# Kernel tuning notes

Measured on AMD Instinct MI355X. Metric: run time of the kernel, lower is better.

The kernel has to match this reference:

```python
import jax, jax.numpy as jnp
import numpy as np

N, E, H, D_IN, L, G, T = 50000, 800000, 64, 64, 4, 128, 1

def _w(key, shape, fan_in):
    return jax.random.normal(key, shape, dtype=jnp.float32) / np.sqrt(fan_in)

def setup_inputs() -> dict:
    key = jax.random.key(0)
    ks = jax.random.split(key, 24)
    inp = {
        'x': jax.random.normal(ks[0], (N, D_IN), dtype=jnp.float32),
        'w': jax.random.normal(ks[1], (E, 1), dtype=jnp.float32),
        'src': jax.random.randint(ks[2], (E,), 0, N, dtype=jnp.int32),
        'dst': jax.random.randint(ks[3], (E,), 0, N, dtype=jnp.int32),
        'graph_id': jnp.sort(jax.random.randint(ks[4], (N,), 0, G, dtype=jnp.int32)),
        # input MLP (1 layer, last_activation None; SiLU applied in input_node_func)
        'W_in': _w(ks[5], (D_IN, H), D_IN), 'b_in': jnp.zeros((H,), jnp.float32),
        # per-layer message MLP: (2H+1 -> H -> H), SiLU mid and last
        'msg_W1': _w(ks[6], (L, 2 * H + 1, H), 2 * H + 1), 'msg_b1': jnp.zeros((L, H), jnp.float32),
        'msg_W2': _w(ks[7], (L, H, H), H), 'msg_b2': jnp.zeros((L, H), jnp.float32),
        # per-layer update MLP: (H -> H -> H), SiLU mid, last None
        'upd_W1': _w(ks[8], (L, H, H), H), 'upd_b1': jnp.zeros((L, H), jnp.float32),
        'upd_W2': _w(ks[9], (L, H, H), H), 'upd_b2': jnp.zeros((L, H), jnp.float32),
        # node-wise output MLP: (H -> H -> H), SiLU mid, last None
        'out_W1': _w(ks[10], (H, H), H), 'out_b1': jnp.zeros((H,), jnp.float32),
        'out_W2': _w(ks[11], (H, H), H), 'out_b2': jnp.zeros((H,), jnp.float32),
        # readout MLP: (3H -> H -> T), SiLU mid, last None
        'ro_W1': _w(ks[12], (3 * H, H), 3 * H), 'ro_b1': jnp.zeros((H,), jnp.float32),
        'ro_W2': _w(ks[13], (H, T), H), 'ro_b2': jnp.zeros((T,), jnp.float32),
    }
    return inp

def reference(x, w, src, dst, graph_id, W_in, b_in, msg_W1, msg_b1, msg_W2, msg_b2,
              upd_W1, upd_b1, upd_W2, upd_b2, out_W1, out_b1, out_W2, out_b2,
              ro_W1, ro_b1, ro_W2, ro_b2):
    silu = jax.nn.silu
    f = silu(x @ W_in + b_in)                                   # [N, H]
    sq = w * w                                                  # [E, 1]
    for l in range(L):
        mi = jnp.concatenate([f[src], f[dst], sq], axis=-1)     # [E, 2H+1]
        msg = silu(silu(mi @ msg_W1[l] + msg_b1[l]) @ msg_W2[l] + msg_b2[l])
        m = msg * jax.nn.sigmoid(msg)                           # gated message
        m_sum = jax.ops.segment_sum(m, dst, num_segments=N)     # scatter-sum to dst
        h_new = silu((m_sum + f) @ upd_W1[l] + upd_b1[l]) @ upd_W2[l] + upd_b2[l]
        f = h_new + f                                           # residual
    f = silu(f @ out_W1 + out_b1) @ out_W2 + out_b2             # node-wise output
    g_sum = jax.ops.segment_sum(f, graph_id, num_segments=G)
    cnt = jax.ops.segment_sum(jnp.ones((N, 1), f.dtype), graph_id, num_segments=G)
    g_mean = g_sum / jnp.maximum(cnt, 1.0)
    g_max = jax.ops.segment_max(f, graph_id, num_segments=G)
    readout = jnp.concatenate([g_sum, g_mean, g_max], axis=-1)  # [G, 3H]
    return silu(readout @ ro_W1 + ro_b1) @ ro_W2 + ro_b2        # [G, T]
```

## Files before the change

### kernel.cpp

```cpp
#include <hip/hip_runtime.h>

#define NN 50000
#define EE 800000
#define GG 128
#define LL 4
#define SCAN_B 196

typedef __bf16 bf16x8 __attribute__((ext_vector_type(8)));
typedef __bf16 bf16x4 __attribute__((ext_vector_type(4)));
typedef float  f32x4  __attribute__((ext_vector_type(4)));

__device__ __forceinline__ float silu_f(float x){
    float t = __builtin_amdgcn_exp2f(-1.44269504f * x);
    return x * __builtin_amdgcn_rcpf(1.0f + t);
}

__global__ __launch_bounds__(256) void pack_k(
        const float* __restrict__ msgW1, const float* __restrict__ msgW2,
        const float* __restrict__ updW1, const float* __restrict__ updW2,
        const float* __restrict__ outW1, const float* __restrict__ outW2,
        const float* __restrict__ W_in, __bf16* __restrict__ pk){
    int m = blockIdx.x;
    const float* src;
    if(m<20){
        int l=m/5, r=m%5;
        if(r==0)      src = msgW1 + (size_t)l*129*64;
        else if(r==1) src = msgW1 + (size_t)l*129*64 + 64*64;
        else if(r==2) src = msgW2 + (size_t)l*64*64;
        else if(r==3) src = updW1 + (size_t)l*64*64;
        else          src = updW2 + (size_t)l*64*64;
    } else if(m==20) src=outW1; else if(m==21) src=outW2; else src=W_in;
    __bf16* dst = pk + (size_t)m*4096;
    int tid=threadIdx.x;
    #pragma unroll
    for(int i=0;i<16;++i){
        int idx = tid*16+i;
        int frag = idx>>9, lane=(idx>>3)&63, j=idx&7;
        int s=frag>>2, ng=frag&3, q=lane>>4, nn=lane&15;
        dst[idx] = (__bf16)src[(32*s+8*q+j)*64 + 16*ng + nn];
    }
}
__device__ __forceinline__ bf16x8 ldfrag(const __bf16* pk, int s, int ng, int lane){
    return *(const bf16x8*)&pk[(((s*4+ng)*64 + lane))*8];
}

__global__ __launch_bounds__(256) void input_mfma(const float* __restrict__ x,
        const __bf16* __restrict__ pkW, const float* __restrict__ bg,
        const __bf16* __restrict__ pkXYa, const __bf16* __restrict__ pkXYb,
        const float* __restrict__ bXY,
        float* __restrict__ f, __bf16* __restrict__ XYout, int N){
    int tid=threadIdx.x, wid=tid>>6, lane=tid&63;
    int q=lane>>4, nn=lane&15;
    bf16x8 Bf[2][4];
    #pragma unroll
    for(int s=0;s<2;++s)
        #pragma unroll
        for(int ng=0;ng<4;++ng) Bf[s][ng]=ldfrag(pkW,s,ng,lane);
    float bias[4], bXYv[4];
    #pragma unroll
    for(int ng=0;ng<4;++ng){ bias[ng]=bg[16*ng+nn]; bXYv[ng]=bXY[16*ng+nn]; }

    __shared__ __align__(16) __bf16 sh1[4][16][72];

    int ntiles=(N+15)/16;
    int gw=gridDim.x*4;
    for(int t=blockIdx.x*4+wid; t<ntiles; t+=gw){
        int m=t*16+nn; int mc=(m<N)?m:(N-1);
        float4 a0=*(const float4*)&x[(size_t)mc*64 + 8*q];
        float4 a1=*(const float4*)&x[(size_t)mc*64 + 8*q + 4];
        float4 a2=*(const float4*)&x[(size_t)mc*64 + 32 + 8*q];
        float4 a3=*(const float4*)&x[(size_t)mc*64 + 32 + 8*q + 4];
        bf16x8 af0, af1;
        af0[0]=(__bf16)a0.x; af0[1]=(__bf16)a0.y; af0[2]=(__bf16)a0.z; af0[3]=(__bf16)a0.w;
        af0[4]=(__bf16)a1.x; af0[5]=(__bf16)a1.y; af0[6]=(__bf16)a1.z; af0[7]=(__bf16)a1.w;
        af1[0]=(__bf16)a2.x; af1[1]=(__bf16)a2.y; af1[2]=(__bf16)a2.z; af1[3]=(__bf16)a2.w;
        af1[4]=(__bf16)a3.x; af1[5]=(__bf16)a3.y; af1[6]=(__bf16)a3.z; af1[7]=(__bf16)a3.w;
        #pragma unroll
        for(int ng=0;ng<4;++ng){
            f32x4 acc; acc[0]=bias[ng]; acc[1]=bias[ng]; acc[2]=bias[ng]; acc[3]=bias[ng];
            acc=__builtin_amdgcn_mfma_f32_16x16x32_bf16(af0,Bf[0][ng],acc,0,0,0);
            acc=__builtin_amdgcn_mfma_f32_16x16x32_bf16(af1,Bf[1][ng],acc,0,0,0);
            #pragma unroll
            for(int r=0;r<4;++r){
                int row=t*16+4*q+r;
                float o=silu_f(acc[r]);
                if(row<N) f[(size_t)row*64+16*ng+nn]=o;
                sh1[wid][4*q+r][16*ng+nn]=(__bf16)o;
            }
        }
        asm volatile("" ::: "memory");
        bf16x8 a30=*(const bf16x8*)&sh1[wid][nn][8*q];
        bf16x8 a31=*(const bf16x8*)&sh1[wid][nn][32+8*q];
        #pragma unroll
        for(int ng=0;ng<8;++ng){
            const __bf16* pkx = (ng<4)? pkXYa : pkXYb;
            int g2 = ng&3;
            float bb = (ng<4)?0.f:bXYv[ng-4];
            f32x4 accx; accx[0]=bb; accx[1]=bb; accx[2]=bb; accx[3]=bb;
            accx=__builtin_amdgcn_mfma_f32_16x16x32_bf16(a30,ldfrag(pkx,0,g2,lane),accx,0,0,0);
            accx=__builtin_amdgcn_mfma_f32_16x16x32_bf16(a31,ldfrag(pkx,1,g2,lane),accx,0,0,0);
            #pragma unroll
            for(int r=0;r<4;++r){
                int row=t*16+4*q+r;
                if(row<N) XYout[(size_t)row*128 + 16*ng + nn]=(__bf16)accx[r];
            }
        }
        asm volatile("" ::: "memory");
    }
}

__global__ void hist_k(const int* __restrict__ dst, int* __restrict__ deg, int E){
    int e=blockIdx.x*blockDim.x+threadIdx.x;
    if(e<E) atomicAdd(&deg[dst[e]],1);
}

__global__ __launch_bounds__(256) void scan1_k(const int* __restrict__ deg, int* __restrict__ curs,
        int* __restrict__ bsum, int N){
    __shared__ int sv[256];
    int tid=threadIdx.x;
    int idx=blockIdx.x*256+tid;
    int v=(idx<N)?deg[idx]:0;
    sv[tid]=v; __syncthreads();
    #pragma unroll
    for(int off=1; off<256; off<<=1){
        int a=(tid>=off)?sv[tid-off]:0;
        __syncthreads(); sv[tid]+=a; __syncthreads();
    }
    if(idx<N) curs[idx]=sv[tid]-v;
    if(tid==255) bsum[blockIdx.x]=sv[255];
}
__global__ __launch_bounds__(256) void scan2_k(int* __restrict__ bsum, int B){
    __shared__ int sv[256];
    int tid=threadIdx.x;
    int v=(tid<B)?bsum[tid]:0;
    sv[tid]=v; __syncthreads();
    #pragma unroll
    for(int off=1; off<256; off<<=1){
        int a=(tid>=off)?sv[tid-off]:0;
        __syncthreads(); sv[tid]+=a; __syncthreads();
    }
    if(tid<B) bsum[tid]=sv[tid]-v;
}
__global__ __launch_bounds__(256) void scan3_k(int* __restrict__ curs, const int* __restrict__ bsum, int N){
    int idx=blockIdx.x*256+threadIdx.x;
    if(idx<N) curs[idx]+=bsum[blockIdx.x];
}

__global__ void fill_k(const int* __restrict__ src, const int* __restrict__ dst,
                       const float* __restrict__ w, int* __restrict__ cursor,
                       int4* __restrict__ meta, int E){
    int e=blockIdx.x*blockDim.x+threadIdx.x;
    if(e<E){
        int d=dst[e];
        int r=atomicAdd(&cursor[d],1);
        float ww=w[e];
        int4 v; v.x=src[e]; v.y=d; v.z=__float_as_int(ww*ww); v.w=0;
        meta[r]=v;
    }
}

__global__ __launch_bounds__(256) void edge_mfma6(
        const __bf16* __restrict__ XY, const int4* __restrict__ meta,
        const __bf16* __restrict__ pkW2,
        const float* __restrict__ W1, const float* __restrict__ b2,
        float* __restrict__ msum, int E){
    int tid=threadIdx.x, wid=tid>>6, lane=tid&63;
    int q=lane>>4, nn=lane&15;

    bf16x8 B2f[2][4];
    #pragma unroll
    for(int s=0;s<2;++s)
        #pragma unroll
        for(int ng=0;ng<4;++ng) B2f[s][ng]=ldfrag(pkW2,s,ng,lane);
    float w128lo[8], w128hi[8];
    #pragma unroll
    for(int j=0;j<8;++j){
        w128lo[j]=W1[128*64 + 8*q+j];
        w128hi[j]=W1[128*64 + 32+8*q+j];
    }
    float bias2[4];
    #pragma unroll
    for(int ng=0;ng<4;++ng) bias2[ng]=b2[16*ng+nn];

    __shared__ __align__(16) __bf16 sm16[4][32][68];
    int cpos = 4*(lane&15) + (lane>>4);

    int ntiles=E/32;
    int nw=gridDim.x*4;
    int chunk=(ntiles+nw-1)/nw;
    int wgl=blockIdx.x*4+wid;
    int t0=wgl*chunk, t1=t0+chunk; if(t1>ntiles) t1=ntiles;
    if(t0>=t1) return;

    int4 mv  = meta[(size_t)t0*32 + (lane&31)];
    int4 mvn = (t0+1<t1) ? meta[(size_t)(t0+1)*32 + (lane&31)] : mv;
    bf16x8 gx0lo,gx0hi,gy0lo,gy0hi,gx1lo,gx1hi,gy1lo,gy1hi;
    {
        int se0=__shfl(mv.x, nn,64),    de0=__shfl(mv.y, nn,64);
        int se1=__shfl(mv.x, 16+nn,64), de1=__shfl(mv.y, 16+nn,64);
        const __bf16* xp0=XY+(size_t)se0*128; const __bf16* yp0=XY+(size_t)de0*128+64;
        const __bf16* xp1=XY+(size_t)se1*128; const __bf16* yp1=XY+(size_t)de1*128+64;
        gx0lo=*(const bf16x8*)(xp0+8*q); gx0hi=*(const bf16x8*)(xp0+32+8*q);
        gy0lo=*(const bf16x8*)(yp0+8*q); gy0hi=*(const bf16x8*)(yp0+32+8*q);
        gx1lo=*(const bf16x8*)(xp1+8*q); gx1hi=*(const bf16x8*)(xp1+32+8*q);
        gy1lo=*(const bf16x8*)(yp1+8*q); gy1hi=*(const bf16x8*)(yp1+32+8*q);
    }
    int cur=__builtin_amdgcn_readlane(mv.y, 0);
    float vsum=0.f;

    for(int t=t0;t<t1;++t){
        int4 mv2 = mvn;
        if(t+2<t1) mv2 = meta[(size_t)(t+2)*32 + (lane&31)];

        int d_ = mv.y;
        float w2v = __int_as_float(mv.z);

        bf16x8 A0lo,A0hi,A1lo,A1hi;
        {
            float w2a = __shfl(w2v, nn, 64);
            float w2b = __shfl(w2v, 16+nn, 64);
            #pragma unroll
            for(int j=0;j<8;++j){
                A0lo[j]=(__bf16)silu_f((float)gx0lo[j] + (float)gy0lo[j] + w2a*w128lo[j]);
                A0hi[j]=(__bf16)silu_f((float)gx0hi[j] + (float)gy0hi[j] + w2a*w128hi[j]);
                A1lo[j]=(__bf16)silu_f((float)gx1lo[j] + (float)gy1lo[j] + w2b*w128lo[j]);
                A1hi[j]=(__bf16)silu_f((float)gx1hi[j] + (float)gy1hi[j] + w2b*w128hi[j]);
            }
        }
        if(t+1<t1){
            int se0=__shfl(mvn.x, nn,64),    de0=__shfl(mvn.y, nn,64);
            int se1=__shfl(mvn.x, 16+nn,64), de1=__shfl(mvn.y, 16+nn,64);
            const __bf16* xp0=XY+(size_t)se0*128; const __bf16* yp0=XY+(size_t)de0*128+64;
            const __bf16* xp1=XY+(size_t)se1*128; const __bf16* yp1=XY+(size_t)de1*128+64;
            gx0lo=*(const bf16x8*)(xp0+8*q); gx0hi=*(const bf16x8*)(xp0+32+8*q);
            gy0lo=*(const bf16x8*)(yp0+8*q); gy0hi=*(const bf16x8*)(yp0+32+8*q);
            gx1lo=*(const bf16x8*)(xp1+8*q); gx1hi=*(const bf16x8*)(xp1+32+8*q);
            gy1lo=*(const bf16x8*)(yp1+8*q); gy1hi=*(const bf16x8*)(yp1+32+8*q);
        }
        #pragma unroll
        for(int h=0;h<2;++h){
            bf16x8 alo = h ? A1lo : A0lo;
            bf16x8 ahi = h ? A1hi : A0hi;
            f32x4 acc2[4];
            #pragma unroll
            for(int ng=0;ng<4;++ng){ f32x4 c; c[0]=bias2[ng]; c[1]=bias2[ng]; c[2]=bias2[ng]; c[3]=bias2[ng]; acc2[ng]=c; }
            #pragma unroll
            for(int ng=0;ng<4;++ng){
                acc2[ng]=__builtin_amdgcn_mfma_f32_16x16x32_bf16(alo,B2f[0][ng],acc2[ng],0,0,0);
                acc2[ng]=__builtin_amdgcn_mfma_f32_16x16x32_bf16(ahi,B2f[1][ng],acc2[ng],0,0,0);
            }
            #pragma unroll
            for(int r=0;r<4;++r){
                bf16x4 pv;
                #pragma unroll
                for(int ng=0;ng<4;++ng) pv[ng]=(__bf16)silu_f(silu_f(acc2[ng][r]));
                *(bf16x4*)&sm16[wid][16*h+4*q+r][4*nn] = pv;
            }
        }
        asm volatile("" ::: "memory");
        {
            int dprev = __shfl(d_, (lane+63)&63, 64);
            unsigned long long bal = __ballot(lane>=1 && lane<32 && d_!=dprev);
            unsigned bmask = (unsigned)bal;
            int d0 = __builtin_amdgcn_readlane(d_, 0);
            if(d0 != cur) bmask |= 1u;
            #pragma unroll
            for(int r=0;r<32;++r){
                if(bmask & (1u<<r)){
                    atomicAdd(&msum[(size_t)cur*64+lane], vsum);
                    vsum=0.f;
                    cur=__builtin_amdgcn_readlane(d_, r);
                }
                vsum += (float)sm16[wid][r][cpos];
            }
        }
        asm volatile("" ::: "memory");
        mv = mvn; mvn = mv2;
    }
    atomicAdd(&msum[(size_t)cur*64+lane], vsum);
}

__global__ __launch_bounds__(256) void node_mfma(float* A, const float* F,
        const __bf16* __restrict__ pkW1, const float* __restrict__ b1,
        const __bf16* __restrict__ pkW2, const float* __restrict__ b2,
        float* __restrict__ out, int zeroA,
        const __bf16* __restrict__ pkXYa, const __bf16* __restrict__ pkXYb,
        const float* __restrict__ bXY, __bf16* __restrict__ XYout, int N){
    int tid=threadIdx.x, wid=tid>>6, lane=tid&63;
    int q=lane>>4, nn=lane&15;

    bf16x8 B1f[2][4], B2f[2][4];
    #pragma unroll
    for(int s=0;s<2;++s)
        #pragma unroll
        for(int ng=0;ng<4;++ng){ B1f[s][ng]=ldfrag(pkW1,s,ng,lane); B2f[s][ng]=ldfrag(pkW2,s,ng,lane); }
    float bias1[4], bias2[4];
    #pragma unroll
    for(int ng=0;ng<4;++ng){ bias1[ng]=b1[16*ng+nn]; bias2[ng]=b2[16*ng+nn]; }
    bool hasXY = (pkXYa != nullptr);
    float bXYv[4];
    #pragma unroll
    for(int j=0;j<4;++j) bXYv[j] = hasXY ? bXY[16*j+nn] : 0.f;

    __shared__ __align__(16) __bf16 sh1[4][16][72];
    __shared__ __align__(16) float sF[4][16][68];
    bool hasF = (F != nullptr);

    int ntiles=(N+15)/16;
    int gw=gridDim.x*4;
    for(int t=blockIdx.x*4+wid; t<ntiles; t+=gw){
        int m=t*16+nn;
        int mc=(m<N)?m:(N-1);
        float4 a0=*(const float4*)&A[(size_t)mc*64 + 8*q];
        float4 a1=*(const float4*)&A[(size_t)mc*64 + 8*q + 4];
        float4 a2=*(const float4*)&A[(size_t)mc*64 + 32 + 8*q];
        float4 a3=*(const float4*)&A[(size_t)mc*64 + 32 + 8*q + 4];
        if(hasF){
            float4 f0=*(const float4*)&F[(size_t)mc*64 + 8*q];
            float4 f1=*(const float4*)&F[(size_t)mc*64 + 8*q + 4];
            float4 f2_=*(const float4*)&F[(size_t)mc*64 + 32 + 8*q];
            float4 f3=*(const float4*)&F[(size_t)mc*64 + 32 + 8*q + 4];
            a0.x+=f0.x; a0.y+=f0.y; a0.z+=f0.z; a0.w+=f0.w;
            a1.x+=f1.x; a1.y+=f1.y; a1.z+=f1.z; a1.w+=f1.w;
            a2.x+=f2_.x; a2.y+=f2_.y; a2.z+=f2_.z; a2.w+=f2_.w;
            a3.x+=f3.x; a3.y+=f3.y; a3.z+=f3.z; a3.w+=f3.w;
            *(float4*)&sF[wid][nn][8*q]   = f0;
            *(float4*)&sF[wid][nn][8*q+4] = f1;
            *(float4*)&sF[wid][nn][32+8*q]   = f2_;
            *(float4*)&sF[wid][nn][32+8*q+4] = f3;
        }
        if(zeroA && m<N){
            float4 z; z.x=0.f; z.y=0.f; z.z=0.f; z.w=0.f;
            *(float4*)&A[(size_t)mc*64 + 8*q]      = z;
            *(float4*)&A[(size_t)mc*64 + 8*q + 4]  = z;
            *(float4*)&A[(size_t)mc*64 + 32 + 8*q] = z;
            *(float4*)&A[(size_t)mc*64 + 32 + 8*q + 4] = z;
        }
        bf16x8 af0, af1;
        af0[0]=(__bf16)a0.x; af0[1]=(__bf16)a0.y; af0[2]=(__bf16)a0.z; af0[3]=(__bf16)a0.w;
        af0[4]=(__bf16)a1.x; af0[5]=(__bf16)a1.y; af0[6]=(__bf16)a1.z; af0[7]=(__bf16)a1.w;
        af1[0]=(__bf16)a2.x; af1[1]=(__bf16)a2.y; af1[2]=(__bf16)a2.z; af1[3]=(__bf16)a2.w;
        af1[4]=(__bf16)a3.x; af1[5]=(__bf16)a3.y; af1[6]=(__bf16)a3.z; af1[7]=(__bf16)a3.w;

        f32x4 acc[4];
        #pragma unroll
        for(int ng=0;ng<4;++ng){ f32x4 c; c[0]=bias1[ng]; c[1]=bias1[ng]; c[2]=bias1[ng]; c[3]=bias1[ng]; acc[ng]=c; }
        #pragma unroll
        for(int ng=0;ng<4;++ng){
            acc[ng]=__builtin_amdgcn_mfma_f32_16x16x32_bf16(af0,B1f[0][ng],acc[ng],0,0,0);
            acc[ng]=__builtin_amdgcn_mfma_f32_16x16x32_bf16(af1,B1f[1][ng],acc[ng],0,0,0);
        }
        #pragma unroll
        for(int ng=0;ng<4;++ng)
            #pragma unroll
            for(int r=0;r<4;++r)
                sh1[wid][4*q+r][16*ng+nn]=(__bf16)silu_f(acc[ng][r]);
        asm volatile("" ::: "memory");
        bf16x8 a20=*(const bf16x8*)&sh1[wid][nn][8*q];
        bf16x8 a21=*(const bf16x8*)&sh1[wid][nn][32+8*q];
        f32x4 acc2[4];
        #pragma unroll
        for(int ng=0;ng<4;++ng){ f32x4 c; c[0]=bias2[ng]; c[1]=bias2[ng]; c[2]=bias2[ng]; c[3]=bias2[ng]; acc2[ng]=c; }
        #pragma unroll
        for(int ng=0;ng<4;++ng){
            acc2[ng]=__builtin_amdgcn_mfma_f32_16x16x32_bf16(a20,B2f[0][ng],acc2[ng],0,0,0);
            acc2[ng]=__builtin_amdgcn_mfma_f32_16x16x32_bf16(a21,B2f[1][ng],acc2[ng],0,0,0);
        }
        #pragma unroll
        for(int ng=0;ng<4;++ng)
            #pragma unroll
            for(int r=0;r<4;++r){
                int row=t*16+4*q+r;
                float o=acc2[ng][r];
                if(hasF) o += sF[wid][4*q+r][16*ng+nn];
                if(row<N) out[(size_t)row*64 + 16*ng + nn]=o;
                if(hasXY) sh1[wid][4*q+r][16*ng+nn]=(__bf16)o;
            }
        asm volatile("" ::: "memory");
        if(hasXY){
            bf16x8 a30=*(const bf16x8*)&sh1[wid][nn][8*q];
            bf16x8 a31=*(const bf16x8*)&sh1[wid][nn][32+8*q];
            #pragma unroll
            for(int ng=0;ng<8;++ng){
                const __bf16* pkx = (ng<4)? pkXYa : pkXYb;
                int g2 = ng&3;
                float bb = (ng<4)?0.f:bXYv[ng-4];
                f32x4 accx; accx[0]=bb; accx[1]=bb; accx[2]=bb; accx[3]=bb;
                accx=__builtin_amdgcn_mfma_f32_16x16x32_bf16(a30,ldfrag(pkx,0,g2,lane),accx,0,0,0);
                accx=__builtin_amdgcn_mfma_f32_16x16x32_bf16(a31,ldfrag(pkx,1,g2,lane),accx,0,0,0);
                #pragma unroll
                for(int r=0;r<4;++r){
                    int row=t*16+4*q+r;
                    if(row<N) XYout[(size_t)row*128 + 16*ng + nn]=(__bf16)accx[r];
                }
            }
        }
        asm volatile("" ::: "memory");
    }
}

__global__ __launch_bounds__(256) void readout_fused(const float* __restrict__ f2,
        const int* __restrict__ gid,
        const float* __restrict__ W1, const float* __restrict__ b1,
        const float* __restrict__ W2, const float* __restrict__ b2,
        float* __restrict__ out, int N, int G){
    __shared__ __align__(16) float sr[4][192];
    int tid=threadIdx.x, wid=tid>>6, lane=tid&63;
    int g=blockIdx.x*4+wid;
    if(g<G){
        int lo=0, hi=N;
        while(lo<hi){ int mid=(lo+hi)>>1; if(gid[mid]<g) lo=mid+1; else hi=mid; }
        int a=lo, b=N;
        while(a<b){ int mid=(a+b)>>1; if(gid[mid]<g+1) a=mid+1; else b=mid; }
        int n0=lo, n1=a;
        float s=0.f, mx=-__builtin_inff();
        int n=n0;
        for(; n+4<=n1; n+=4){
            float v0=f2[(size_t)(n+0)*64+lane];
            float v1=f2[(size_t)(n+1)*64+lane];
            float v2=f2[(size_t)(n+2)*64+lane];
            float v3=f2[(size_t)(n+3)*64+lane];
            s += (v0+v1)+(v2+v3);
            mx = fmaxf(mx, fmaxf(fmaxf(v0,v1), fmaxf(v2,v3)));
        }
        for(; n<n1; ++n){ float v=f2[(size_t)n*64+lane]; s+=v; mx=fmaxf(mx,v); }
        float c=(float)(n1-n0);
        float mean=s/fmaxf(c,1.0f);
        sr[wid][lane]=s; sr[wid][64+lane]=mean; sr[wid][128+lane]=mx;
    }
    __syncthreads();
    if(g<G){
        float h=b1[lane];
        for(int k=0;k<192;k+=4){
            float4 r4=*(const float4*)&sr[wid][k];
            h += r4.x*W1[(k+0)*64+lane] + r4.y*W1[(k+1)*64+lane]
               + r4.z*W1[(k+2)*64+lane] + r4.w*W1[(k+3)*64+lane];
        }
        h=silu_f(h);
        float p=h*W2[lane];
        #pragma unroll
        for(int off=32;off>0;off>>=1) p += __shfl_down(p, off, 64);
        if(lane==0) out[g]=p+b2[0];
    }
}

extern "C" void kernel_launch(void* const* d_in, const int* in_sizes, int n_in,
                              void* d_out, int out_size, void* d_ws, size_t ws_size,
                              hipStream_t stream){
    const float* x     = (const float*)d_in[0];
    const float* w     = (const float*)d_in[1];
    const int*   src   = (const int*)d_in[2];
    const int*   dst   = (const int*)d_in[3];
    const int*   gid   = (const int*)d_in[4];
    const float* W_in  = (const float*)d_in[5];
    const float* b_in  = (const float*)d_in[6];
    const float* msgW1 = (const float*)d_in[7];
    const float* msgb1 = (const float*)d_in[8];
    const float* msgW2 = (const float*)d_in[9];
    const float* msgb2 = (const float*)d_in[10];
    const float* updW1 = (const float*)d_in[11];
    const float* updb1 = (const float*)d_in[12];
    const float* updW2 = (const float*)d_in[13];
    const float* updb2 = (const float*)d_in[14];
    const float* outW1 = (const float*)d_in[15];
    const float* outb1 = (const float*)d_in[16];
    const float* outW2 = (const float*)d_in[17];
    const float* outb2 = (const float*)d_in[18];
    const float* roW1  = (const float*)d_in[19];
    const float* rob1  = (const float*)d_in[20];
    const float* roW2  = (const float*)d_in[21];
    const float* rob2  = (const float*)d_in[22];

    float*  f     = (float*)d_ws;
    float*  msum  = f + (size_t)NN*64;
    float*  f2    = msum;
    __bf16* XY    = (__bf16*)(msum + (size_t)NN*64);
    int4*   meta  = (int4*)(XY + (size_t)NN*128);
    __bf16* pk    = (__bf16*)(meta + EE);
    int*    deg   = (int*)(pk + 23*4096);
    int*    curs  = deg + 50048;
    int*    bsum  = curs + 50048;

    pack_k<<<dim3(23),dim3(256),0,stream>>>(msgW1, msgW2, updW1, updW2, outW1, outW2, W_in, pk);

    hipMemsetAsync(deg, 0, 50048*sizeof(int), stream);
    hist_k<<<dim3((EE+255)/256),dim3(256),0,stream>>>(dst, deg, EE);
    scan1_k<<<dim3(SCAN_B),dim3(256),0,stream>>>(deg, curs, bsum, NN);
    scan2_k<<<dim3(1),dim3(256),0,stream>>>(bsum, SCAN_B);
    scan3_k<<<dim3(SCAN_B),dim3(256),0,stream>>>(curs, bsum, NN);
    fill_k<<<dim3((EE+255)/256),dim3(256),0,stream>>>(src, dst, w, curs, meta, EE);

    hipMemsetAsync(msum, 0, (size_t)NN*64*sizeof(float), stream);
    input_mfma<<<dim3(782),dim3(256),0,stream>>>(x, pk + (size_t)22*4096, b_in,
        pk + (size_t)0*4096, pk + (size_t)1*4096, msgb1 + 0*64, f, XY, NN);
    for(int l=0;l<LL;++l){
        edge_mfma6<<<dim3(1280),dim3(256),0,stream>>>(XY, meta,
            pk + (size_t)(5*l+2)*4096,
            msgW1 + (size_t)l*129*64, msgb2 + l*64, msum, EE);
        bool fuse = (l < LL-1);
        node_mfma<<<dim3(782),dim3(256),0,stream>>>(msum, f,
            pk + (size_t)(5*l+3)*4096, updb1 + l*64,
            pk + (size_t)(5*l+4)*4096, updb2 + l*64, f, 1,
            fuse ? pk + (size_t)(5*(l+1)+0)*4096 : nullptr,
            fuse ? pk + (size_t)(5*(l+1)+1)*4096 : nullptr,
            fuse ? msgb1 + (l+1)*64 : nullptr,
            XY, NN);
    }
    node_mfma<<<dim3(782),dim3(256),0,stream>>>(f, nullptr,
        pk + (size_t)20*4096, outb1, pk + (size_t)21*4096, outb2, f2, 0,
        nullptr, nullptr, nullptr, nullptr, NN);
    readout_fused<<<dim3(32),dim3(256),0,stream>>>(f2, gid, roW1, rob1, roW2, rob2,
        (float*)d_out, NN, GG);
}
```

Baseline: 562.7 us.

## Split graph readout into a parallel segmented reduction with atomics

```diff
diff --git a/kernel.cpp b/kernel.cpp
--- a/kernel.cpp
+++ b/kernel.cpp
@@ -13,6 +13,13 @@
 __device__ __forceinline__ float silu_f(float x){
     float t = __builtin_amdgcn_exp2f(-1.44269504f * x);
     return x * __builtin_amdgcn_rcpf(1.0f + t);
+}
+__device__ __forceinline__ unsigned fenc(float v){
+    unsigned u = __float_as_uint(v);
+    return (u & 0x80000000u) ? ~u : (u | 0x80000000u);
+}
+__device__ __forceinline__ float fdec(unsigned u){
+    return (u & 0x80000000u) ? __uint_as_float(u & 0x7fffffffu) : __uint_as_float(~u);
 }
 
 __global__ __launch_bounds__(256) void pack_k(
@@ -399,34 +406,47 @@
     }
 }
 
-__global__ __launch_bounds__(256) void readout_fused(const float* __restrict__ f2,
-        const int* __restrict__ gid,
+__global__ __launch_bounds__(256) void seg_reduce_sorted(const float* __restrict__ f2, const int* __restrict__ gid,
+        float* __restrict__ gsum, unsigned* __restrict__ gmaxu, float* __restrict__ cnt, int N){
+    int wgl=blockIdx.x*4 + (threadIdx.x>>6);
+    int lane=threadIdx.x&63;
+    int W=gridDim.x*4;
+    int chunk=(N+W-1)/W;
+    int n0=wgl*chunk;
+    int n1=n0+chunk; if(n1>N) n1=N;
+    if(n0>=n1) return;
+    int cur=gid[n0];
+    float s=0.f, mx=-__builtin_inff(), c=0.f;
+    for(int n=n0;n<n1;++n){
+        int g=gid[n];
+        float v=f2[(size_t)n*64+lane];
+        if(g!=cur){
+            atomicAdd(&gsum[(size_t)cur*64+lane], s);
+            atomicMax(&gmaxu[(size_t)cur*64+lane], fenc(mx));
+            if(lane==0) atomicAdd(&cnt[cur], c);
+            s=0.f; mx=-__builtin_inff(); c=0.f; cur=g;
+        }
+        s+=v; mx=fmaxf(mx,v); c+=1.f;
+    }
+    atomicAdd(&gsum[(size_t)cur*64+lane], s);
+    atomicMax(&gmaxu[(size_t)cur*64+lane], fenc(mx));
+    if(lane==0) atomicAdd(&cnt[cur], c);
+}
+
+__global__ __launch_bounds__(256) void readout_k(const float* __restrict__ gsum, const unsigned* __restrict__ gmaxu,
+        const float* __restrict__ cnt,
         const float* __restrict__ W1, const float* __restrict__ b1,
         const float* __restrict__ W2, const float* __restrict__ b2,
-        float* __restrict__ out, int N, int G){
+        float* __restrict__ out, int G){
     __shared__ __align__(16) float sr[4][192];
     int tid=threadIdx.x, wid=tid>>6, lane=tid&63;
     int g=blockIdx.x*4+wid;
     if(g<G){
-        int lo=0, hi=N;
-        while(lo<hi){ int mid=(lo+hi)>>1; if(gid[mid]<g) lo=mid+1; else hi=mid; }
-        int a=lo, b=N;
-        while(a<b){ int mid=(a+b)>>1; if(gid[mid]<g+1) a=mid+1; else b=mid; }
-        int n0=lo, n1=a;
-        float s=0.f, mx=-__builtin_inff();
-        int n=n0;
-        for(; n+4<=n1; n+=4){
-            float v0=f2[(size_t)(n+0)*64+lane];
-            float v1=f2[(size_t)(n+1)*64+lane];
-            float v2=f2[(size_t)(n+2)*64+lane];
-            float v3=f2[(size_t)(n+3)*64+lane];
-            s += (v0+v1)+(v2+v3);
-            mx = fmaxf(mx, fmaxf(fmaxf(v0,v1), fmaxf(v2,v3)));
-        }
-        for(; n<n1; ++n){ float v=f2[(size_t)n*64+lane]; s+=v; mx=fmaxf(mx,v); }
-        float c=(float)(n1-n0);
-        float mean=s/fmaxf(c,1.0f);
-        sr[wid][lane]=s; sr[wid][64+lane]=mean; sr[wid][128+lane]=mx;
+        float s_=gsum[g*64+lane];
+        float c=cnt[g];
+        float mean=s_/fmaxf(c,1.0f);
+        float mx=fdec(gmaxu[g*64+lane]);
+        sr[wid][lane]=s_; sr[wid][64+lane]=mean; sr[wid][128+lane]=mx;
     }
     __syncthreads();
     if(g<G){
@@ -480,6 +500,9 @@
     int*    deg   = (int*)(pk + 23*4096);
     int*    curs  = deg + 50048;
     int*    bsum  = curs + 50048;
+    float*  gsum  = (float*)(bsum + 256);
+    unsigned* gmaxu = (unsigned*)(gsum + GG*64);
+    float*  cnt   = (float*)(gmaxu + GG*64);
 
     pack_k<<<dim3(23),dim3(256),0,stream>>>(msgW1, msgW2, updW1, updW2, outW1, outW2, W_in, pk);
 
@@ -509,6 +532,7 @@
     node_mfma<<<dim3(782),dim3(256),0,stream>>>(f, nullptr,
         pk + (size_t)20*4096, outb1, pk + (size_t)21*4096, outb2, f2, 0,
         nullptr, nullptr, nullptr, nullptr, NN);
-    readout_fused<<<dim3(32),dim3(256),0,stream>>>(f2, gid, roW1, rob1, roW2, rob2,
-        (float*)d_out, NN, GG);
-}
+    hipMemsetAsync(gsum, 0, (size_t)(GG*64*2 + GG)*sizeof(float), stream);
+    seg_reduce_sorted<<<dim3(256),dim3(256),0,stream>>>(f2, gid, gsum, gmaxu, cnt, NN);
+    readout_k<<<dim3(32),dim3(256),0,stream>>>(gsum, gmaxu, cnt, roW1, rob1, roW2, rob2, (float*)d_out, GG);
+}
```

After: 538.1 us, median of 2. 1.05x faster.
